# Kernel optimization log

Measured on AMD Instinct MI355X. Metric: run time of the kernel, lower is better.

The kernel has to match this reference:

```python
import jax, jax.numpy as jnp
import numpy as np

TP = 4
TOKENS = 8192
HIDDEN = 4096
EPS = 1e-6
FP8_MAX = 448.0  # float8_e4m3fn max


def setup_inputs() -> dict:
    key = jax.random.key(0)
    k1, k2, k3 = jax.random.split(key, 3)
    hidden_states = jax.random.normal(k1, (TP, TOKENS, HIDDEN), dtype=jnp.float32)
    residual = jax.random.normal(k2, (TOKENS, HIDDEN), dtype=jnp.float32)
    weight = jax.random.uniform(k3, (HIDDEN,), dtype=jnp.float32)
    return {"hidden_states": hidden_states, "residual": residual, "weight": weight}


def rms_norm(x, weight, eps):
    # vLLM RMSNorm: x * rsqrt(mean(x^2) + eps) * weight, computed in fp32
    var = jnp.mean(jnp.square(x), axis=-1, keepdims=True)
    return x * jax.lax.rsqrt(var + eps) * weight


def scaled_fp8_quant(x):
    # dynamic per-tensor fp8 quantization: scale = amax / FP8_MAX
    amax = jnp.max(jnp.abs(x))
    scale = jnp.maximum(amax, 1e-12) / FP8_MAX
    q = jnp.clip(x / scale, -FP8_MAX, FP8_MAX)  # quantized values (kept fp32 for reference math)
    return q, scale


def reference(hidden_states, residual, weight):
    # tensor_model_parallel_all_reduce == sum over TP shards (leading axis)
    all_reduce = jnp.sum(hidden_states, axis=0)  # [TOKENS, HIDDEN]
    normed = rms_norm(all_reduce, weight, EPS)
    q, scale = scaled_fp8_quant(normed)
    return q, scale
```

## Files before the change

### kernel.cpp

```cpp
#include <hip/hip_runtime.h>
#include <hip/hip_fp16.h>

#define TP_ 4
#define TOKENS_ 8192
#define HIDDEN_ 4096
#define EPS_ 1e-6f
#define FP8MAX_ 448.0f

typedef float f32x4 __attribute__((ext_vector_type(4)));
typedef unsigned int u32x4 __attribute__((ext_vector_type(4)));

static constexpr size_t NELEM = (size_t)TOKENS_ * HIDDEN_;
static constexpr size_t WS_SCALE_OFF = 0;
static constexpr size_t WS_BMAX_OFF = 4096;
static constexpr size_t WS_H16_OFF = 65536;
static constexpr size_t WS_NEEDED = WS_H16_OFF + NELEM * sizeof(unsigned short);

static __device__ inline unsigned int pack_half2(float a, float b) {
    __half2 h = __floats2half2_rn(a, b);
    return *reinterpret_cast<unsigned int*>(&h);
}

__global__ __launch_bounds__(256) void k_norm_h(
    const float* __restrict__ hs, const float* __restrict__ w,
    unsigned int* __restrict__ normed_h2, float* __restrict__ bmax_arr)
{
    const int row = blockIdx.x;
    const int tid = threadIdx.x;
    const size_t S4 = NELEM / 4;
    const f32x4* __restrict__ base =
        reinterpret_cast<const f32x4*>(hs) + (size_t)row * (HIDDEN_ / 4);
    const f32x4* __restrict__ w4 = reinterpret_cast<const f32x4*>(w);

    f32x4 sv[4];
    float ss = 0.f;
#pragma unroll
    for (int j = 0; j < 4; ++j) {
        const size_t idx = (size_t)tid + j * 256;
        f32x4 a = __builtin_nontemporal_load(&base[idx]);
        f32x4 b = __builtin_nontemporal_load(&base[idx + S4]);
        f32x4 c = __builtin_nontemporal_load(&base[idx + 2 * S4]);
        f32x4 d = __builtin_nontemporal_load(&base[idx + 3 * S4]);
        f32x4 s = (a + b) + (c + d);
        sv[j] = s;
        ss += s.x * s.x + s.y * s.y + s.z * s.z + s.w * s.w;
    }

    __shared__ float red[4];
#pragma unroll
    for (int off = 32; off > 0; off >>= 1) ss += __shfl_down(ss, off, 64);
    const int wave = tid >> 6;
    if ((tid & 63) == 0) red[wave] = ss;
    __syncthreads();
    ss = red[0] + red[1] + red[2] + red[3];
    const float inv = rsqrtf(ss * (1.0f / HIDDEN_) + EPS_);

    uint2* __restrict__ out =
        reinterpret_cast<uint2*>(normed_h2) + (size_t)row * (HIDDEN_ / 4);
    float am = 0.f;
#pragma unroll
    for (int j = 0; j < 4; ++j) {
        const size_t idx = (size_t)tid + j * 256;
        f32x4 wv = w4[idx];
        f32x4 s = sv[j];
        f32x4 o = s * inv * wv;
        uint2 p;
        p.x = pack_half2(o.x, o.y);
        p.y = pack_half2(o.z, o.w);
        out[idx] = p;
        am = fmaxf(am, fmaxf(fmaxf(fabsf(o.x), fabsf(o.y)),
                             fmaxf(fabsf(o.z), fabsf(o.w))));
    }

    __shared__ float redm[4];
#pragma unroll
    for (int off = 32; off > 0; off >>= 1)
        am = fmaxf(am, __shfl_down(am, off, 64));
    if ((tid & 63) == 0) redm[wave] = am;
    __syncthreads();
    if (tid == 0)
        bmax_arr[row] = fmaxf(fmaxf(redm[0], redm[1]), fmaxf(redm[2], redm[3]));
}

__global__ __launch_bounds__(256) void k_amax_scale(
    const float* __restrict__ bmax_arr, float* __restrict__ ws_scale,
    float* __restrict__ scale_out)
{
    const int tid = threadIdx.x;
    const f32x4* __restrict__ b4 = reinterpret_cast<const f32x4*>(bmax_arr);
    float am = 0.f;
#pragma unroll
    for (int j = 0; j < 8; ++j) {
        f32x4 v = b4[tid + j * 256];
        am = fmaxf(am, fmaxf(fmaxf(v.x, v.y), fmaxf(v.z, v.w)));
    }
    __shared__ float red[4];
#pragma unroll
    for (int off = 32; off > 0; off >>= 1)
        am = fmaxf(am, __shfl_down(am, off, 64));
    if ((tid & 63) == 0) red[tid >> 6] = am;
    __syncthreads();
    if (tid == 0) {
        am = fmaxf(fmaxf(red[0], red[1]), fmaxf(red[2], red[3]));
        const float scale = fmaxf(am, 1e-12f) / FP8MAX_;
        ws_scale[0] = scale;
        scale_out[0] = scale;
    }
}

__global__ __launch_bounds__(256) void k_quant_h(
    const unsigned int* __restrict__ normed_h2,
    const float* __restrict__ ws_scale, float* __restrict__ q_out)
{
    const float invs = 1.0f / ws_scale[0];
    const size_t n8 = NELEM / 8;
    const u32x4* __restrict__ src = reinterpret_cast<const u32x4*>(normed_h2);
    f32x4* __restrict__ dst = reinterpret_cast<f32x4*>(q_out);
    const size_t stride = (size_t)gridDim.x * blockDim.x;
    for (size_t i = (size_t)blockIdx.x * blockDim.x + threadIdx.x; i < n8;
         i += stride) {
        u32x4 u = src[i];
        unsigned int u0 = u.x, u1 = u.y, u2 = u.z, u3 = u.w;
        float2 f0 = __half22float2(*reinterpret_cast<const __half2*>(&u0));
        float2 f1 = __half22float2(*reinterpret_cast<const __half2*>(&u1));
        float2 f2 = __half22float2(*reinterpret_cast<const __half2*>(&u2));
        float2 f3 = __half22float2(*reinterpret_cast<const __half2*>(&u3));
        f32x4 a, b;
        a.x = fminf(fmaxf(f0.x * invs, -FP8MAX_), FP8MAX_);
        a.y = fminf(fmaxf(f0.y * invs, -FP8MAX_), FP8MAX_);
        a.z = fminf(fmaxf(f1.x * invs, -FP8MAX_), FP8MAX_);
        a.w = fminf(fmaxf(f1.y * invs, -FP8MAX_), FP8MAX_);
        b.x = fminf(fmaxf(f2.x * invs, -FP8MAX_), FP8MAX_);
        b.y = fminf(fmaxf(f2.y * invs, -FP8MAX_), FP8MAX_);
        b.z = fminf(fmaxf(f3.x * invs, -FP8MAX_), FP8MAX_);
        b.w = fminf(fmaxf(f3.y * invs, -FP8MAX_), FP8MAX_);
        __builtin_nontemporal_store(a, &dst[i * 2]);
        __builtin_nontemporal_store(b, &dst[i * 2 + 1]);
    }
}


__global__ __launch_bounds__(256) void k_fused_norm_f(
    const float* __restrict__ hs, const float* __restrict__ w,
    float* __restrict__ normed, float* __restrict__ bmax_arr)
{
    const int row = blockIdx.x;
    const int tid = threadIdx.x;
    const size_t S4 = NELEM / 4;
    const f32x4* __restrict__ base =
        reinterpret_cast<const f32x4*>(hs) + (size_t)row * (HIDDEN_ / 4);
    const f32x4* __restrict__ w4 = reinterpret_cast<const f32x4*>(w);
    f32x4 sv[4];
    float ss = 0.f;
#pragma unroll
    for (int j = 0; j < 4; ++j) {
        const size_t idx = (size_t)tid + j * 256;
        f32x4 a = base[idx];
        f32x4 b = base[idx + S4];
        f32x4 c = base[idx + 2 * S4];
        f32x4 d = base[idx + 3 * S4];
        f32x4 s = (a + b) + (c + d);
        sv[j] = s;
        ss += s.x * s.x + s.y * s.y + s.z * s.z + s.w * s.w;
    }
    __shared__ float red[4];
#pragma unroll
    for (int off = 32; off > 0; off >>= 1) ss += __shfl_down(ss, off, 64);
    const int wave = tid >> 6;
    if ((tid & 63) == 0) red[wave] = ss;
    __syncthreads();
    ss = red[0] + red[1] + red[2] + red[3];
    const float inv = rsqrtf(ss * (1.0f / HIDDEN_) + EPS_);
    f32x4* __restrict__ out =
        reinterpret_cast<f32x4*>(normed) + (size_t)row * (HIDDEN_ / 4);
    float am = 0.f;
#pragma unroll
    for (int j = 0; j < 4; ++j) {
        const size_t idx = (size_t)tid + j * 256;
        f32x4 wv = w4[idx];
        f32x4 o = sv[j] * inv * wv;
        out[idx] = o;
        am = fmaxf(am, fmaxf(fmaxf(fabsf(o.x), fabsf(o.y)),
                             fmaxf(fabsf(o.z), fabsf(o.w))));
    }
    __shared__ float redm[4];
#pragma unroll
    for (int off = 32; off > 0; off >>= 1)
        am = fmaxf(am, __shfl_down(am, off, 64));
    if ((tid & 63) == 0) redm[wave] = am;
    __syncthreads();
    if (tid == 0)
        bmax_arr[row] = fmaxf(fmaxf(redm[0], redm[1]), fmaxf(redm[2], redm[3]));
}

__global__ __launch_bounds__(256) void k_quant_f(
    float* __restrict__ data, const float* __restrict__ ws_scale)
{
    const float invs = 1.0f / ws_scale[0];
    const size_t n4 = NELEM / 4;
    f32x4* __restrict__ d4 = reinterpret_cast<f32x4*>(data);
    const size_t stride = (size_t)gridDim.x * blockDim.x;
    for (size_t i = (size_t)blockIdx.x * blockDim.x + threadIdx.x; i < n4;
         i += stride) {
        f32x4 v = d4[i];
        v.x = fminf(fmaxf(v.x * invs, -FP8MAX_), FP8MAX_);
        v.y = fminf(fmaxf(v.y * invs, -FP8MAX_), FP8MAX_);
        v.z = fminf(fmaxf(v.z * invs, -FP8MAX_), FP8MAX_);
        v.w = fminf(fmaxf(v.w * invs, -FP8MAX_), FP8MAX_);
        d4[i] = v;
    }
}

extern "C" void kernel_launch(void* const* d_in, const int* in_sizes, int n_in,
                              void* d_out, int out_size, void* d_ws, size_t ws_size,
                              hipStream_t stream) {
    const float* hs = (const float*)d_in[0];
    const float* w  = (const float*)d_in[2];
    float* out = (float*)d_out;
    float* scale_out = out + NELEM;

    float* ws_scale = (float*)((char*)d_ws + WS_SCALE_OFF);
    float* bmax_arr = (float*)((char*)d_ws + WS_BMAX_OFF);

    if (ws_size >= WS_NEEDED) {
        unsigned int* normed_h2 = (unsigned int*)((char*)d_ws + WS_H16_OFF);
        k_norm_h<<<TOKENS_, 256, 0, stream>>>(hs, w, normed_h2, bmax_arr);
        k_amax_scale<<<1, 256, 0, stream>>>(bmax_arr, ws_scale, scale_out);
        k_quant_h<<<2048, 256, 0, stream>>>(normed_h2, ws_scale, out);
    } else {
        k_fused_norm_f<<<TOKENS_, 256, 0, stream>>>(hs, w, out, bmax_arr);
        k_amax_scale<<<1, 256, 0, stream>>>(bmax_arr, ws_scale, scale_out);
        k_quant_f<<<2048, 256, 0, stream>>>(out, ws_scale);
    }
}
```

Before: 152.2 us.

## Fuse norm, amax and quant into one cooperative kernel with register-held fp16 rows

Replaces the three-kernel pipeline with one cooperative kernel of 1024 blocks, each handling 8 rows. Each block keeps its normalized values packed as fp16 in registers, synchronizes the whole grid to get the global amax, then quantizes and writes the output directly. This removes the fp16 intermediate round trip through global memory and two extra kernel launches. The cost is high register use (64 packed words per thread), possibly lower occupancy, and a grid-wide barrier. If the cooperative launch fails it falls back to the old three-kernel path, and the fp32 fallback for small workspaces is removed.

Measured after the change: 332.1 us. +118.2%, slower.

```diff
diff --git a/kernel.cpp b/kernel.cpp
--- a/kernel.cpp
+++ b/kernel.cpp
@@ -1,7 +1,9 @@
 #include <hip/hip_runtime.h>
 #include <hip/hip_fp16.h>
-
-#define TP_ 4
+#include <hip/hip_cooperative_groups.h>
+
+namespace cg = cooperative_groups;
+
 #define TOKENS_ 8192
 #define HIDDEN_ 4096
 #define EPS_ 1e-6f
@@ -14,12 +16,122 @@
 static constexpr size_t WS_SCALE_OFF = 0;
 static constexpr size_t WS_BMAX_OFF = 4096;
 static constexpr size_t WS_H16_OFF = 65536;
-static constexpr size_t WS_NEEDED = WS_H16_OFF + NELEM * sizeof(unsigned short);
+static constexpr size_t WS_NEEDED_FB = WS_H16_OFF + NELEM * sizeof(unsigned short);
 
 static __device__ inline unsigned int pack_half2(float a, float b) {
     __half2 h = __floats2half2_rn(a, b);
     return *reinterpret_cast<unsigned int*>(&h);
 }
+static __device__ inline float2 unpack_half2(unsigned int u) {
+    return __half22float2(*reinterpret_cast<const __half2*>(&u));
+}
+static __device__ inline float clip1(float x, float invs) {
+    return fminf(fmaxf(x * invs, -FP8MAX_), FP8MAX_);
+}
+
+__global__ __launch_bounds__(256, 4) void k_coop(
+    const float* __restrict__ hs, const float* __restrict__ w,
+    float* __restrict__ q_out, float* __restrict__ scale_out,
+    float* __restrict__ bmax_arr)
+{
+    const int tid = threadIdx.x;
+    const int wave = tid >> 6;
+    const int row0 = blockIdx.x * 8;
+    const size_t S4 = NELEM / 4;
+    const f32x4* __restrict__ w4 = reinterpret_cast<const f32x4*>(w);
+
+    unsigned int pk[64];
+    float bmax = 0.f;
+    __shared__ float red[32];
+
+#define ROW_J(R, J, SV)                                                       \
+    {                                                                         \
+        f32x4 a = __builtin_nontemporal_load(&base[tid + J * 256]);           \
+        f32x4 b = __builtin_nontemporal_load(&base[tid + J * 256 + S4]);      \
+        f32x4 c = __builtin_nontemporal_load(&base[tid + J * 256 + 2 * S4]);  \
+        f32x4 d = __builtin_nontemporal_load(&base[tid + J * 256 + 3 * S4]);  \
+        SV = (a + b) + (c + d);                                               \
+        ss += SV.x * SV.x + SV.y * SV.y + SV.z * SV.z + SV.w * SV.w;          \
+    }
+
+#define ROW_O(R, J, SV)                                                       \
+    {                                                                         \
+        f32x4 wv = w4[tid + J * 256];                                         \
+        f32x4 o = SV * inv * wv;                                              \
+        pk[R * 8 + J * 2]     = pack_half2(o.x, o.y);                         \
+        pk[R * 8 + J * 2 + 1] = pack_half2(o.z, o.w);                         \
+        bmax = fmaxf(bmax, fmaxf(fmaxf(fabsf(o.x), fabsf(o.y)),               \
+                                 fmaxf(fabsf(o.z), fabsf(o.w))));             \
+    }
+
+#define DO_ROW(R)                                                             \
+    {                                                                         \
+        const f32x4* __restrict__ base =                                      \
+            reinterpret_cast<const f32x4*>(hs) +                              \
+            (size_t)(row0 + R) * (HIDDEN_ / 4);                               \
+        f32x4 sv0, sv1, sv2, sv3;                                             \
+        float ss = 0.f;                                                       \
+        ROW_J(R, 0, sv0) ROW_J(R, 1, sv1) ROW_J(R, 2, sv2) ROW_J(R, 3, sv3)   \
+        for (int off = 32; off > 0; off >>= 1)                                \
+            ss += __shfl_down(ss, off, 64);                                   \
+        if ((tid & 63) == 0) red[R * 4 + wave] = ss;                          \
+        __syncthreads();                                                      \
+        ss = red[R * 4 + 0] + red[R * 4 + 1] + red[R * 4 + 2] +               \
+             red[R * 4 + 3];                                                  \
+        const float inv = rsqrtf(ss * (1.0f / HIDDEN_) + EPS_);               \
+        ROW_O(R, 0, sv0) ROW_O(R, 1, sv1) ROW_O(R, 2, sv2) ROW_O(R, 3, sv3)   \
+    }
+
+    DO_ROW(0) DO_ROW(1) DO_ROW(2) DO_ROW(3)
+    DO_ROW(4) DO_ROW(5) DO_ROW(6) DO_ROW(7)
+
+    for (int off = 32; off > 0; off >>= 1)
+        bmax = fmaxf(bmax, __shfl_down(bmax, off, 64));
+    if ((tid & 63) == 0) red[wave] = bmax;
+    __syncthreads();
+    if (tid == 0) {
+        bmax_arr[blockIdx.x] =
+            fmaxf(fmaxf(red[0], red[1]), fmaxf(red[2], red[3]));
+        __threadfence();
+    }
+
+    cg::this_grid().sync();
+
+    f32x4 bv = reinterpret_cast<const f32x4*>(bmax_arr)[tid];
+    float am = fmaxf(fmaxf(bv.x, bv.y), fmaxf(bv.z, bv.w));
+    for (int off = 32; off > 0; off >>= 1)
+        am = fmaxf(am, __shfl_down(am, off, 64));
+    __syncthreads();
+    if ((tid & 63) == 0) red[wave] = am;
+    __syncthreads();
+    am = fmaxf(fmaxf(red[0], red[1]), fmaxf(red[2], red[3]));
+    const float scale = fmaxf(am, 1e-12f) / FP8MAX_;
+    const float invs = 1.0f / scale;
+    if (blockIdx.x == 0 && tid == 0) scale_out[0] = scale;
+
+#define ST_J(R, J)                                                            \
+    {                                                                         \
+        float2 f0 = unpack_half2(pk[R * 8 + J * 2]);                          \
+        float2 f1 = unpack_half2(pk[R * 8 + J * 2 + 1]);                      \
+        f32x4 o;                                                              \
+        o.x = clip1(f0.x, invs);                                              \
+        o.y = clip1(f0.y, invs);                                              \
+        o.z = clip1(f1.x, invs);                                              \
+        o.w = clip1(f1.y, invs);                                              \
+        __builtin_nontemporal_store(o, &dst[tid + J * 256]);                  \
+    }
+
+#define ST_ROW(R)                                                             \
+    {                                                                         \
+        f32x4* __restrict__ dst = reinterpret_cast<f32x4*>(q_out) +           \
+                                  (size_t)(row0 + R) * (HIDDEN_ / 4);         \
+        ST_J(R, 0) ST_J(R, 1) ST_J(R, 2) ST_J(R, 3)                           \
+    }
+
+    ST_ROW(0) ST_ROW(1) ST_ROW(2) ST_ROW(3)
+    ST_ROW(4) ST_ROW(5) ST_ROW(6) ST_ROW(7)
+}
+
 
 __global__ __launch_bounds__(256) void k_norm_h(
     const float* __restrict__ hs, const float* __restrict__ w,
@@ -45,7 +157,6 @@
         sv[j] = s;
         ss += s.x * s.x + s.y * s.y + s.z * s.z + s.w * s.w;
     }
-
     __shared__ float red[4];
 #pragma unroll
     for (int off = 32; off > 0; off >>= 1) ss += __shfl_down(ss, off, 64);
@@ -62,8 +173,7 @@
     for (int j = 0; j < 4; ++j) {
         const size_t idx = (size_t)tid + j * 256;
         f32x4 wv = w4[idx];
-        f32x4 s = sv[j];
-        f32x4 o = s * inv * wv;
+        f32x4 o = sv[j] * inv * wv;
         uint2 p;
         p.x = pack_half2(o.x, o.y);
         p.y = pack_half2(o.z, o.w);
@@ -71,7 +181,6 @@
         am = fmaxf(am, fmaxf(fmaxf(fabsf(o.x), fabsf(o.y)),
                              fmaxf(fabsf(o.z), fabsf(o.w))));
     }
-
     __shared__ float redm[4];
 #pragma unroll
     for (int off = 32; off > 0; off >>= 1)
@@ -120,94 +229,21 @@
     for (size_t i = (size_t)blockIdx.x * blockDim.x + threadIdx.x; i < n8;
          i += stride) {
         u32x4 u = src[i];
-        unsigned int u0 = u.x, u1 = u.y, u2 = u.z, u3 = u.w;
-        float2 f0 = __half22float2(*reinterpret_cast<const __half2*>(&u0));
-        float2 f1 = __half22float2(*reinterpret_cast<const __half2*>(&u1));
-        float2 f2 = __half22float2(*reinterpret_cast<const __half2*>(&u2));
-        float2 f3 = __half22float2(*reinterpret_cast<const __half2*>(&u3));
+        float2 f0 = unpack_half2(u.x);
+        float2 f1 = unpack_half2(u.y);
+        float2 f2 = unpack_half2(u.z);
+        float2 f3 = unpack_half2(u.w);
         f32x4 a, b;
-        a.x = fminf(fmaxf(f0.x * invs, -FP8MAX_), FP8MAX_);
-        a.y = fminf(fmaxf(f0.y * invs, -FP8MAX_), FP8MAX_);
-        a.z = fminf(fmaxf(f1.x * invs, -FP8MAX_), FP8MAX_);
-        a.w = fminf(fmaxf(f1.y * invs, -FP8MAX_), FP8MAX_);
-        b.x = fminf(fmaxf(f2.x * invs, -FP8MAX_), FP8MAX_);
-        b.y = fminf(fmaxf(f2.y * invs, -FP8MAX_), FP8MAX_);
-        b.z = fminf(fmaxf(f3.x * invs, -FP8MAX_), FP8MAX_);
-        b.w = fminf(fmaxf(f3.y * invs, -FP8MAX_), FP8MAX_);
+        a.x = clip1(f0.x, invs);
+        a.y = clip1(f0.y, invs);
+        a.z = clip1(f1.x, invs);
+        a.w = clip1(f1.y, invs);
+        b.x = clip1(f2.x, invs);
+        b.y = clip1(f2.y, invs);
+        b.z = clip1(f3.x, invs);
+        b.w = clip1(f3.y, invs);
         __builtin_nontemporal_store(a, &dst[i * 2]);
         __builtin_nontemporal_store(b, &dst[i * 2 + 1]);
-    }
-}
-
-
-__global__ __launch_bounds__(256) void k_fused_norm_f(
-    const float* __restrict__ hs, const float* __restrict__ w,
-    float* __restrict__ normed, float* __restrict__ bmax_arr)
-{
-    const int row = blockIdx.x;
-    const int tid = threadIdx.x;
-    const size_t S4 = NELEM / 4;
-    const f32x4* __restrict__ base =
-        reinterpret_cast<const f32x4*>(hs) + (size_t)row * (HIDDEN_ / 4);
-    const f32x4* __restrict__ w4 = reinterpret_cast<const f32x4*>(w);
-    f32x4 sv[4];
-    float ss = 0.f;
-#pragma unroll
-    for (int j = 0; j < 4; ++j) {
-        const size_t idx = (size_t)tid + j * 256;
-        f32x4 a = base[idx];
-        f32x4 b = base[idx + S4];
-        f32x4 c = base[idx + 2 * S4];
-        f32x4 d = base[idx + 3 * S4];
-        f32x4 s = (a + b) + (c + d);
-        sv[j] = s;
-        ss += s.x * s.x + s.y * s.y + s.z * s.z + s.w * s.w;
-    }
-    __shared__ float red[4];
-#pragma unroll
-    for (int off = 32; off > 0; off >>= 1) ss += __shfl_down(ss, off, 64);
-    const int wave = tid >> 6;
-    if ((tid & 63) == 0) red[wave] = ss;
-    __syncthreads();
-    ss = red[0] + red[1] + red[2] + red[3];
-    const float inv = rsqrtf(ss * (1.0f / HIDDEN_) + EPS_);
-    f32x4* __restrict__ out =
-        reinterpret_cast<f32x4*>(normed) + (size_t)row * (HIDDEN_ / 4);
-    float am = 0.f;
-#pragma unroll
-    for (int j = 0; j < 4; ++j) {
-        const size_t idx = (size_t)tid + j * 256;
-        f32x4 wv = w4[idx];
-        f32x4 o = sv[j] * inv * wv;
-        out[idx] = o;
-        am = fmaxf(am, fmaxf(fmaxf(fabsf(o.x), fabsf(o.y)),
-                             fmaxf(fabsf(o.z), fabsf(o.w))));
-    }
-    __shared__ float redm[4];
-#pragma unroll
-    for (int off = 32; off > 0; off >>= 1)
-        am = fmaxf(am, __shfl_down(am, off, 64));
-    if ((tid & 63) == 0) redm[wave] = am;
-    __syncthreads();
-    if (tid == 0)
-        bmax_arr[row] = fmaxf(fmaxf(redm[0], redm[1]), fmaxf(redm[2], redm[3]));
-}
-
-__global__ __launch_bounds__(256) void k_quant_f(
-    float* __restrict__ data, const float* __restrict__ ws_scale)
-{
-    const float invs = 1.0f / ws_scale[0];
-    const size_t n4 = NELEM / 4;
-    f32x4* __restrict__ d4 = reinterpret_cast<f32x4*>(data);
-    const size_t stride = (size_t)gridDim.x * blockDim.x;
-    for (size_t i = (size_t)blockIdx.x * blockDim.x + threadIdx.x; i < n4;
-         i += stride) {
-        f32x4 v = d4[i];
-        v.x = fminf(fmaxf(v.x * invs, -FP8MAX_), FP8MAX_);
-        v.y = fminf(fmaxf(v.y * invs, -FP8MAX_), FP8MAX_);
-        v.z = fminf(fmaxf(v.z * invs, -FP8MAX_), FP8MAX_);
-        v.w = fminf(fmaxf(v.w * invs, -FP8MAX_), FP8MAX_);
-        d4[i] = v;
     }
 }
 
@@ -222,14 +258,14 @@
     float* ws_scale = (float*)((char*)d_ws + WS_SCALE_OFF);
     float* bmax_arr = (float*)((char*)d_ws + WS_BMAX_OFF);
 
-    if (ws_size >= WS_NEEDED) {
+    void* args[] = {(void*)&hs, (void*)&w, (void*)&out, (void*)&scale_out,
+                    (void*)&bmax_arr};
+    hipError_t err = hipLaunchCooperativeKernel(
+        (const void*)k_coop, dim3(1024), dim3(256), args, 0, stream);
+    if (err != hipSuccess && ws_size >= WS_NEEDED_FB) {
         unsigned int* normed_h2 = (unsigned int*)((char*)d_ws + WS_H16_OFF);
         k_norm_h<<<TOKENS_, 256, 0, stream>>>(hs, w, normed_h2, bmax_arr);
         k_amax_scale<<<1, 256, 0, stream>>>(bmax_arr, ws_scale, scale_out);
         k_quant_h<<<2048, 256, 0, stream>>>(normed_h2, ws_scale, out);
-    } else {
-        k_fused_norm_f<<<TOKENS_, 256, 0, stream>>>(hs, w, out, bmax_arr);
-        k_amax_scale<<<1, 256, 0, stream>>>(bmax_arr, ws_scale, scale_out);
-        k_quant_f<<<2048, 256, 0, stream>>>(out, ws_scale);
-    }
-}
+    }
+}
```
